# Kernel optimization log

Hardware: AMD Instinct MI355X
Metric: run time of the kernel (lower is better)

Reference implementation:

```python
import jax, jax.numpy as jnp
import numpy as np

N, NA, F = 16384, 256, 2048
GAMMA = 1.5
BN_EPS = 1e-5


def setup_inputs() -> dict:
    key = jax.random.key(0)
    k1, k2, k3, k4, k5 = jax.random.split(key, 5)
    a = jax.random.normal(k1, (N, NA), dtype=jnp.float32)
    ps = jax.random.uniform(k2, (N, F), dtype=jnp.float32)
    lim = 1.0 / np.sqrt(NA)
    W = jax.random.uniform(k3, (F, NA), minval=-lim, maxval=lim, dtype=jnp.float32)
    b = jax.random.uniform(k4, (F,), minval=-lim, maxval=lim, dtype=jnp.float32)
    bn_w = jnp.ones((F,), dtype=jnp.float32)
    bn_b = jnp.zeros((F,), dtype=jnp.float32)
    return {"a": a, "ps": ps, "W": W, "b": b, "bn_w": bn_w, "bn_b": bn_b}


def sparsemax(z):
    # Faithful translation of the repo's Sparsemax (note: it sorts ASCENDING,
    # exactly as the original torch code does).
    D = z.shape[-1]
    s = jnp.sort(z, axis=-1)                      # ascending, [N, D]
    r = jnp.arange(D, dtype=z.dtype)              # [D]
    w = (1.0 + r * s - jnp.cumsum(s, axis=-1) > 0).astype(jnp.int32)
    k_z = jnp.max(jnp.arange(D, dtype=jnp.int32) * w, axis=-1)   # [N]
    m = (jnp.arange(D)[None, :] < (k_z + 1)[:, None]).astype(z.dtype)  # [N, D]
    m_z = jnp.sum(m * s, axis=-1)                 # [N]
    tau_z = (m_z + 1.0) / k_z.astype(z.dtype)     # [N]
    return jnp.maximum(z - tau_z[:, None], 0.0)


def reference(a, ps, W, b, bn_w, bn_b):
    # Linear: (N, n_a) -> (N, F)
    x = a @ W.T + b
    # BatchNorm1d (training mode: batch statistics, biased variance)
    mu = jnp.mean(x, axis=0)
    var = jnp.mean((x - mu) ** 2, axis=0)
    x = (x - mu) / jnp.sqrt(var + BN_EPS) * bn_w + bn_b
    # Sparsemax over prior-scaled activations
    m = sparsemax(x * ps)
    new_ps = ps * (GAMMA - jax.lax.stop_gradient(m))
    return m, new_ps
```

## Files before the change

kernel.cpp:

```cpp
#include <hip/hip_runtime.h>
#include <hip/hip_bf16.h>
#include <math.h>

#define N_ROWS 16384
#define N_A    256
#define N_F    2048
#define GAMMA  1.5f
#define BN_EPS 1e-5f

typedef __attribute__((ext_vector_type(8))) short short8;
typedef __attribute__((ext_vector_type(4))) float f32x4;

__global__ __launch_bounds__(256) void cvt_bf16(const float* __restrict__ in,
                                                unsigned short* __restrict__ out,
                                                int n4) {
    int i = blockIdx.x * 256 + threadIdx.x;
    if (i >= n4) return;
    float4 v = reinterpret_cast<const float4*>(in)[i];
    ushort4 o;
    o.x = __builtin_bit_cast(unsigned short, __float2bfloat16(v.x));
    o.y = __builtin_bit_cast(unsigned short, __float2bfloat16(v.y));
    o.z = __builtin_bit_cast(unsigned short, __float2bfloat16(v.z));
    o.w = __builtin_bit_cast(unsigned short, __float2bfloat16(v.w));
    reinterpret_cast<ushort4*>(out)[i] = o;
}

__global__ __launch_bounds__(256) void gemm_x(const unsigned short* __restrict__ aB,
                                              const unsigned short* __restrict__ wB,
                                              const float* __restrict__ bias,
                                              unsigned short* __restrict__ xB,
                                              float* __restrict__ ps1,
                                              float* __restrict__ ps2) {
    const int lane = threadIdx.x & 63;
    const int wave = threadIdx.x >> 6;
    const int r16  = lane & 15;
    const int quad = lane >> 4;
    const int col0 = blockIdx.x * 128;
    const int rowB = blockIdx.y * 128;
    const int row0 = rowB + wave * 32;

    f32x4 acc[2][8];
    #pragma unroll
    for (int g = 0; g < 2; ++g)
        #pragma unroll
        for (int t = 0; t < 8; ++t)
            acc[g][t] = (f32x4){0.f, 0.f, 0.f, 0.f};

    const unsigned short* aR0 = aB + (size_t)(row0 + r16) * N_A;
    const unsigned short* aR1 = aR0 + 16 * N_A;
    const unsigned short* wR  = wB + (size_t)(col0 + r16) * N_A;

    #pragma unroll
    for (int ks = 0; ks < 8; ++ks) {
        const int k0 = ks * 32 + quad * 8;
        short8 a0 = *reinterpret_cast<const short8*>(aR0 + k0);
        short8 a1 = *reinterpret_cast<const short8*>(aR1 + k0);
        #pragma unroll
        for (int t = 0; t < 8; ++t) {
            short8 bf = *reinterpret_cast<const short8*>(wR + (size_t)t * 16 * N_A + k0);
            acc[0][t] = __builtin_amdgcn_mfma_f32_16x16x32_bf16(a0, bf, acc[0][t], 0, 0, 0);
            acc[1][t] = __builtin_amdgcn_mfma_f32_16x16x32_bf16(a1, bf, acc[1][t], 0, 0, 0);
        }
    }

    __shared__ float cs1[4][128];
    __shared__ float cs2[4][128];
    __shared__ unsigned short tile[128][136];

    #pragma unroll
    for (int t = 0; t < 8; ++t) {
        const float bcol = bias[col0 + t * 16 + r16];
        float s1 = 0.f, s2 = 0.f;
        #pragma unroll
        for (int g = 0; g < 2; ++g) {
            #pragma unroll
            for (int r = 0; r < 4; ++r) {
                float v = acc[g][t][r] + bcol;
                s1 += v;
                s2 += v * v;
                tile[wave * 32 + g * 16 + quad * 4 + r][t * 16 + r16] =
                    __builtin_bit_cast(unsigned short, __float2bfloat16(v));
            }
        }
        s1 += __shfl_xor(s1, 16); s1 += __shfl_xor(s1, 32);
        s2 += __shfl_xor(s2, 16); s2 += __shfl_xor(s2, 32);
        if (quad == 0) { cs1[wave][t * 16 + r16] = s1; cs2[wave][t * 16 + r16] = s2; }
    }
    __syncthreads();

    if (threadIdx.x < 128) {
        const int c = threadIdx.x;
        float s1 = cs1[0][c] + cs1[1][c] + cs1[2][c] + cs1[3][c];
        float s2 = cs2[0][c] + cs2[1][c] + cs2[2][c] + cs2[3][c];
        ps1[(size_t)blockIdx.y * N_F + col0 + c] = s1;
        ps2[(size_t)blockIdx.y * N_F + col0 + c] = s2;
    }

    {
        const int r = threadIdx.x >> 1;
        const int h = threadIdx.x & 1;
        const unsigned short* src = &tile[r][h * 64];
        unsigned short* dst = xB + (size_t)(rowB + r) * 4096 + col0 + h * 64;
        #pragma unroll
        for (int i = 0; i < 8; ++i)
            *reinterpret_cast<short8*>(dst + i * 8) =
                *reinterpret_cast<const short8*>(src + i * 8);
    }
}

__global__ __launch_bounds__(256) void finalize_stats(const float* __restrict__ ps1,
                                                      const float* __restrict__ ps2,
                                                      const float* __restrict__ bn_w,
                                                      const float* __restrict__ bn_b,
                                                      float* __restrict__ scale,
                                                      float* __restrict__ shift) {
    const int f = blockIdx.x * 256 + threadIdx.x;
    float s1 = 0.f, s2 = 0.f;
    #pragma unroll 4
    for (int i = 0; i < 128; ++i) {
        s1 += ps1[(size_t)i * N_F + f];
        s2 += ps2[(size_t)i * N_F + f];
    }
    const float inv_n = 1.0f / (float)N_ROWS;
    const float mu  = s1 * inv_n;
    const float var = s2 * inv_n - mu * mu;
    const float sc  = bn_w[f] / sqrtf(var + BN_EPS);
    scale[f] = sc;
    shift[f] = bn_b[f] - mu * sc;
}

__global__ __launch_bounds__(256) void bn_sparsemax(const unsigned short* xB,
                                                    const float* __restrict__ ps,
                                                    const float* __restrict__ scale,
                                                    const float* __restrict__ shift,
                                                    float* m_out,
                                                    float* __restrict__ ps_out) {
    const int row = blockIdx.x;
    const int tid = threadIdx.x;
    const int f0  = tid * 8;

    const unsigned short* xr = xB + (size_t)row * 4096 + f0;
    const float* pr = ps + (size_t)row * N_F + f0;

    short8 xv = *reinterpret_cast<const short8*>(xr);
    float4 p0  = *reinterpret_cast<const float4*>(pr);
    float4 p1  = *reinterpret_cast<const float4*>(pr + 4);
    float4 sc0 = *reinterpret_cast<const float4*>(scale + f0);
    float4 sc1 = *reinterpret_cast<const float4*>(scale + f0 + 4);
    float4 sh0 = *reinterpret_cast<const float4*>(shift + f0);
    float4 sh1 = *reinterpret_cast<const float4*>(shift + f0 + 4);

    float pv[8]  = {p0.x, p0.y, p0.z, p0.w, p1.x, p1.y, p1.z, p1.w};
    float scv[8] = {sc0.x, sc0.y, sc0.z, sc0.w, sc1.x, sc1.y, sc1.z, sc1.w};
    float shv[8] = {sh0.x, sh0.y, sh0.z, sh0.w, sh1.x, sh1.y, sh1.z, sh1.w};

    float z[8];
    float s = 0.f, mx = -INFINITY, mn = INFINITY;
    #pragma unroll
    for (int i = 0; i < 8; ++i) {
        float xf = __builtin_bit_cast(float,
                       (unsigned int)((unsigned short)xv[i]) << 16);
        float zz = (xf * scv[i] + shv[i]) * pv[i];
        z[i] = zz;
        s += zz;
        mx = fmaxf(mx, zz);
        mn = fminf(mn, zz);
    }

    #pragma unroll
    for (int off = 32; off > 0; off >>= 1) {
        s  += __shfl_xor(s, off);
        mx  = fmaxf(mx, __shfl_xor(mx, off));
        mn  = fminf(mn, __shfl_xor(mn, off));
    }
    __shared__ float rs[4], rmx[4], rmn[4];
    const int wave = tid >> 6;
    if ((tid & 63) == 0) { rs[wave] = s; rmx[wave] = mx; rmn[wave] = mn; }
    __syncthreads();
    s  = rs[0] + rs[1] + rs[2] + rs[3];
    mx = fmaxf(fmaxf(rmx[0], rmx[1]), fmaxf(rmx[2], rmx[3]));
    mn = fminf(fminf(rmn[0], rmn[1]), fminf(rmn[2], rmn[3]));

    const float c_last = 1.0f + (float)(N_F - 1) * mx - s;
    float tau;
    if (c_last > 0.0f) {
        tau = (s + 1.0f) / (float)(N_F - 1);
    } else {
        tau = (mn + 1.0f) / 0.0f;
    }

    float* mo = m_out  + (size_t)row * N_F + f0;
    float* po = ps_out + (size_t)row * N_F + f0;
    float4 mv0, mv1, po0, po1;
    mv0.x = fmaxf(z[0] - tau, 0.f); po0.x = pv[0] * (GAMMA - mv0.x);
    mv0.y = fmaxf(z[1] - tau, 0.f); po0.y = pv[1] * (GAMMA - mv0.y);
    mv0.z = fmaxf(z[2] - tau, 0.f); po0.z = pv[2] * (GAMMA - mv0.z);
    mv0.w = fmaxf(z[3] - tau, 0.f); po0.w = pv[3] * (GAMMA - mv0.w);
    mv1.x = fmaxf(z[4] - tau, 0.f); po1.x = pv[4] * (GAMMA - mv1.x);
    mv1.y = fmaxf(z[5] - tau, 0.f); po1.y = pv[5] * (GAMMA - mv1.y);
    mv1.z = fmaxf(z[6] - tau, 0.f); po1.z = pv[6] * (GAMMA - mv1.z);
    mv1.w = fmaxf(z[7] - tau, 0.f); po1.w = pv[7] * (GAMMA - mv1.w);
    *reinterpret_cast<float4*>(mo)     = mv0;
    *reinterpret_cast<float4*>(mo + 4) = mv1;
    *reinterpret_cast<float4*>(po)     = po0;
    *reinterpret_cast<float4*>(po + 4) = po1;
}

extern "C" void kernel_launch(void* const* d_in, const int* in_sizes, int n_in,
                              void* d_out, int out_size, void* d_ws, size_t ws_size,
                              hipStream_t stream) {
    const float* a    = (const float*)d_in[0];
    const float* ps   = (const float*)d_in[1];
    const float* W    = (const float*)d_in[2];
    const float* bias = (const float*)d_in[3];
    const float* bnw  = (const float*)d_in[4];
    const float* bnb  = (const float*)d_in[5];

    float* out    = (float*)d_out;
    float* m_out  = out;
    float* ps_out = out + (size_t)N_ROWS * N_F;
    unsigned short* xB = (unsigned short*)d_out;

    char* ws = (char*)d_ws;
    unsigned short* aB = (unsigned short*)ws;
    unsigned short* wB = (unsigned short*)(ws + (8u << 20));
    float* ps1   = (float*)(ws + (9u  << 20));
    float* ps2   = (float*)(ws + (10u << 20));
    float* scale = (float*)(ws + (11u << 20));
    float* shift = (float*)(ws + (11u << 20) + 8192);

    cvt_bf16<<<4096, 256, 0, stream>>>(a, aB, N_ROWS * N_A / 4);
    cvt_bf16<<<512, 256, 0, stream>>>(W, wB, N_F * N_A / 4);
    gemm_x<<<dim3(N_F / 128, N_ROWS / 128), 256, 0, stream>>>(aB, wB, bias, xB, ps1, ps2);
    finalize_stats<<<N_F / 256, 256, 0, stream>>>(ps1, ps2, bnw, bnb, scale, shift);
    bn_sparsemax<<<N_ROWS, 256, 0, stream>>>(xB, ps, scale, shift, m_out, ps_out);
}
```

Measured before the change: 493.4 us.

## Recompute GEMM inside the sparsemax kernel instead of storing bf16 activations

The first GEMM pass now computes only the per-column batch-norm statistics and no longer writes the bf16 activation matrix. A new fused kernel recomputes the GEMM for 16-row blocks, applies batch-norm and the prior scaling, reduces each row for the sparsemax threshold, and writes both outputs directly. This removes a full round trip of the intermediate activation tensor through global memory. The cost is doing the GEMM twice, and the output and ps accesses use narrower, less vectorized per-lane patterns than the old row-per-block kernel.

```diff
diff --git a/kernel.cpp b/kernel.cpp
--- a/kernel.cpp
+++ b/kernel.cpp
@@ -25,12 +25,11 @@
     reinterpret_cast<ushort4*>(out)[i] = o;
 }
 
-__global__ __launch_bounds__(256) void gemm_x(const unsigned short* __restrict__ aB,
-                                              const unsigned short* __restrict__ wB,
-                                              const float* __restrict__ bias,
-                                              unsigned short* __restrict__ xB,
-                                              float* __restrict__ ps1,
-                                              float* __restrict__ ps2) {
+__global__ __launch_bounds__(256) void gemm_stats(const unsigned short* __restrict__ aB,
+                                                  const unsigned short* __restrict__ wB,
+                                                  const float* __restrict__ bias,
+                                                  float* __restrict__ ps1,
+                                                  float* __restrict__ ps2) {
     const int lane = threadIdx.x & 63;
     const int wave = threadIdx.x >> 6;
     const int r16  = lane & 15;
@@ -65,7 +64,6 @@
 
     __shared__ float cs1[4][128];
     __shared__ float cs2[4][128];
-    __shared__ unsigned short tile[128][136];
 
     #pragma unroll
     for (int t = 0; t < 8; ++t) {
@@ -78,8 +76,6 @@
                 float v = acc[g][t][r] + bcol;
                 s1 += v;
                 s2 += v * v;
-                tile[wave * 32 + g * 16 + quad * 4 + r][t * 16 + r16] =
-                    __builtin_bit_cast(unsigned short, __float2bfloat16(v));
             }
         }
         s1 += __shfl_xor(s1, 16); s1 += __shfl_xor(s1, 32);
@@ -94,17 +90,6 @@
         float s2 = cs2[0][c] + cs2[1][c] + cs2[2][c] + cs2[3][c];
         ps1[(size_t)blockIdx.y * N_F + col0 + c] = s1;
         ps2[(size_t)blockIdx.y * N_F + col0 + c] = s2;
-    }
-
-    {
-        const int r = threadIdx.x >> 1;
-        const int h = threadIdx.x & 1;
-        const unsigned short* src = &tile[r][h * 64];
-        unsigned short* dst = xB + (size_t)(rowB + r) * 4096 + col0 + h * 64;
-        #pragma unroll
-        for (int i = 0; i < 8; ++i)
-            *reinterpret_cast<short8*>(dst + i * 8) =
-                *reinterpret_cast<const short8*>(src + i * 8);
     }
 }
 
@@ -129,81 +114,110 @@
     shift[f] = bn_b[f] - mu * sc;
 }
 
-__global__ __launch_bounds__(256) void bn_sparsemax(const unsigned short* xB,
-                                                    const float* __restrict__ ps,
-                                                    const float* __restrict__ scale,
-                                                    const float* __restrict__ shift,
-                                                    float* m_out,
-                                                    float* __restrict__ ps_out) {
-    const int row = blockIdx.x;
-    const int tid = threadIdx.x;
-    const int f0  = tid * 8;
-
-    const unsigned short* xr = xB + (size_t)row * 4096 + f0;
-    const float* pr = ps + (size_t)row * N_F + f0;
-
-    short8 xv = *reinterpret_cast<const short8*>(xr);
-    float4 p0  = *reinterpret_cast<const float4*>(pr);
-    float4 p1  = *reinterpret_cast<const float4*>(pr + 4);
-    float4 sc0 = *reinterpret_cast<const float4*>(scale + f0);
-    float4 sc1 = *reinterpret_cast<const float4*>(scale + f0 + 4);
-    float4 sh0 = *reinterpret_cast<const float4*>(shift + f0);
-    float4 sh1 = *reinterpret_cast<const float4*>(shift + f0 + 4);
-
-    float pv[8]  = {p0.x, p0.y, p0.z, p0.w, p1.x, p1.y, p1.z, p1.w};
-    float scv[8] = {sc0.x, sc0.y, sc0.z, sc0.w, sc1.x, sc1.y, sc1.z, sc1.w};
-    float shv[8] = {sh0.x, sh0.y, sh0.z, sh0.w, sh1.x, sh1.y, sh1.z, sh1.w};
-
-    float z[8];
-    float s = 0.f, mx = -INFINITY, mn = INFINITY;
-    #pragma unroll
-    for (int i = 0; i < 8; ++i) {
-        float xf = __builtin_bit_cast(float,
-                       (unsigned int)((unsigned short)xv[i]) << 16);
-        float zz = (xf * scv[i] + shv[i]) * pv[i];
-        z[i] = zz;
-        s += zz;
-        mx = fmaxf(mx, zz);
-        mn = fminf(mn, zz);
-    }
-
-    #pragma unroll
-    for (int off = 32; off > 0; off >>= 1) {
-        s  += __shfl_xor(s, off);
-        mx  = fmaxf(mx, __shfl_xor(mx, off));
-        mn  = fminf(mn, __shfl_xor(mn, off));
-    }
-    __shared__ float rs[4], rmx[4], rmn[4];
-    const int wave = tid >> 6;
-    if ((tid & 63) == 0) { rs[wave] = s; rmx[wave] = mx; rmn[wave] = mn; }
+__global__ __launch_bounds__(512) void fused_gemm_bn_sparsemax(
+    const unsigned short* __restrict__ aB,
+    const unsigned short* __restrict__ wB,
+    const float* __restrict__ bias,
+    const float* __restrict__ ps,
+    const float* __restrict__ scale,
+    const float* __restrict__ shift,
+    float* __restrict__ m_out,
+    float* __restrict__ ps_out) {
+    const int lane = threadIdx.x & 63;
+    const int wave = threadIdx.x >> 6;
+    const int r16  = lane & 15;
+    const int quad = lane >> 4;
+    const int row0 = blockIdx.x * 16;
+    const int c0   = wave * 256;
+
+    f32x4 acc[16];
+    #pragma unroll
+    for (int t = 0; t < 16; ++t)
+        acc[t] = (f32x4){0.f, 0.f, 0.f, 0.f};
+
+    const unsigned short* aR = aB + (size_t)(row0 + r16) * N_A;
+    const unsigned short* wR = wB + (size_t)(c0 + r16) * N_A;
+
+    #pragma unroll
+    for (int ks = 0; ks < 8; ++ks) {
+        const int k0 = ks * 32 + quad * 8;
+        short8 a0 = *reinterpret_cast<const short8*>(aR + k0);
+        #pragma unroll
+        for (int t = 0; t < 16; ++t) {
+            short8 bf = *reinterpret_cast<const short8*>(wR + (size_t)t * 16 * N_A + k0);
+            acc[t] = __builtin_amdgcn_mfma_f32_16x16x32_bf16(a0, bf, acc[t], 0, 0, 0);
+        }
+    }
+
+    float sp[4]  = {0.f, 0.f, 0.f, 0.f};
+    float mxp[4] = {-INFINITY, -INFINITY, -INFINITY, -INFINITY};
+    float mnp[4] = {INFINITY, INFINITY, INFINITY, INFINITY};
+    #pragma unroll
+    for (int t = 0; t < 16; ++t) {
+        const int col = c0 + t * 16 + r16;
+        const float bcol = bias[col];
+        const float sc   = scale[col];
+        const float sh   = shift[col];
+        #pragma unroll
+        for (int r = 0; r < 4; ++r) {
+            const int row = row0 + quad * 4 + r;
+            const float p = ps[(size_t)row * N_F + col];
+            const float v = acc[t][r] + bcol;
+            const float z = (v * sc + sh) * p;
+            acc[t][r] = z;
+            sp[r]  += z;
+            mxp[r]  = fmaxf(mxp[r], z);
+            mnp[r]  = fminf(mnp[r], z);
+        }
+    }
+    #pragma unroll
+    for (int off = 1; off < 16; off <<= 1) {
+        #pragma unroll
+        for (int r = 0; r < 4; ++r) {
+            sp[r]  += __shfl_xor(sp[r], off);
+            mxp[r]  = fmaxf(mxp[r], __shfl_xor(mxp[r], off));
+            mnp[r]  = fminf(mnp[r], __shfl_xor(mnp[r], off));
+        }
+    }
+
+    __shared__ float red_s[16][8], red_mx[16][8], red_mn[16][8];
+    __shared__ float tau_s[16];
+    if (r16 == 0) {
+        #pragma unroll
+        for (int r = 0; r < 4; ++r) {
+            red_s[quad * 4 + r][wave]  = sp[r];
+            red_mx[quad * 4 + r][wave] = mxp[r];
+            red_mn[quad * 4 + r][wave] = mnp[r];
+        }
+    }
     __syncthreads();
-    s  = rs[0] + rs[1] + rs[2] + rs[3];
-    mx = fmaxf(fmaxf(rmx[0], rmx[1]), fmaxf(rmx[2], rmx[3]));
-    mn = fminf(fminf(rmn[0], rmn[1]), fminf(rmn[2], rmn[3]));
-
-    const float c_last = 1.0f + (float)(N_F - 1) * mx - s;
-    float tau;
-    if (c_last > 0.0f) {
-        tau = (s + 1.0f) / (float)(N_F - 1);
-    } else {
-        tau = (mn + 1.0f) / 0.0f;
-    }
-
-    float* mo = m_out  + (size_t)row * N_F + f0;
-    float* po = ps_out + (size_t)row * N_F + f0;
-    float4 mv0, mv1, po0, po1;
-    mv0.x = fmaxf(z[0] - tau, 0.f); po0.x = pv[0] * (GAMMA - mv0.x);
-    mv0.y = fmaxf(z[1] - tau, 0.f); po0.y = pv[1] * (GAMMA - mv0.y);
-    mv0.z = fmaxf(z[2] - tau, 0.f); po0.z = pv[2] * (GAMMA - mv0.z);
-    mv0.w = fmaxf(z[3] - tau, 0.f); po0.w = pv[3] * (GAMMA - mv0.w);
-    mv1.x = fmaxf(z[4] - tau, 0.f); po1.x = pv[4] * (GAMMA - mv1.x);
-    mv1.y = fmaxf(z[5] - tau, 0.f); po1.y = pv[5] * (GAMMA - mv1.y);
-    mv1.z = fmaxf(z[6] - tau, 0.f); po1.z = pv[6] * (GAMMA - mv1.z);
-    mv1.w = fmaxf(z[7] - tau, 0.f); po1.w = pv[7] * (GAMMA - mv1.w);
-    *reinterpret_cast<float4*>(mo)     = mv0;
-    *reinterpret_cast<float4*>(mo + 4) = mv1;
-    *reinterpret_cast<float4*>(po)     = po0;
-    *reinterpret_cast<float4*>(po + 4) = po1;
+    if (threadIdx.x < 16) {
+        float s = 0.f, mx = -INFINITY, mn = INFINITY;
+        #pragma unroll
+        for (int w = 0; w < 8; ++w) {
+            s += red_s[threadIdx.x][w];
+            mx = fmaxf(mx, red_mx[threadIdx.x][w]);
+            mn = fminf(mn, red_mn[threadIdx.x][w]);
+        }
+        const float c_last = 1.0f + (float)(N_F - 1) * mx - s;
+        tau_s[threadIdx.x] = (c_last > 0.0f) ? (s + 1.0f) / (float)(N_F - 1)
+                                             : (mn + 1.0f) / 0.0f;
+    }
+    __syncthreads();
+
+    #pragma unroll
+    for (int t = 0; t < 16; ++t) {
+        const int col = c0 + t * 16 + r16;
+        #pragma unroll
+        for (int r = 0; r < 4; ++r) {
+            const int row = row0 + quad * 4 + r;
+            const float tau = tau_s[quad * 4 + r];
+            const float p   = ps[(size_t)row * N_F + col];
+            const float m   = fmaxf(acc[t][r] - tau, 0.f);
+            m_out[(size_t)row * N_F + col]  = m;
+            ps_out[(size_t)row * N_F + col] = p * (GAMMA - m);
+        }
+    }
 }
 
 extern "C" void kernel_launch(void* const* d_in, const int* in_sizes, int n_in,
@@ -219,7 +233,6 @@
     float* out    = (float*)d_out;
     float* m_out  = out;
     float* ps_out = out + (size_t)N_ROWS * N_F;
-    unsigned short* xB = (unsigned short*)d_out;
 
     char* ws = (char*)d_ws;
     unsigned short* aB = (unsigned short*)ws;
@@ -231,7 +244,8 @@
 
     cvt_bf16<<<4096, 256, 0, stream>>>(a, aB, N_ROWS * N_A / 4);
     cvt_bf16<<<512, 256, 0, stream>>>(W, wB, N_F * N_A / 4);
-    gemm_x<<<dim3(N_F / 128, N_ROWS / 128), 256, 0, stream>>>(aB, wB, bias, xB, ps1, ps2);
+    gemm_stats<<<dim3(N_F / 128, N_ROWS / 128), 256, 0, stream>>>(aB, wB, bias, ps1, ps2);
     finalize_stats<<<N_F / 256, 256, 0, stream>>>(ps1, ps2, bnw, bnb, scale, shift);
-    bn_sparsemax<<<N_ROWS, 256, 0, stream>>>(xB, ps, scale, shift, m_out, ps_out);
-}
+    fused_gemm_bn_sparsemax<<<N_ROWS / 16, 512, 0, stream>>>(aB, wB, bias, ps, scale,
+                                                             shift, m_out, ps_out);
+}
```

New measurement: 715.9 us. +45.1%, slower.
